# Optimization experiments

Hardware: AMD Instinct MI355X
Metric: run time of the kernel (lower is better)

Reference implementation:

```python
import jax, jax.numpy as jnp
import numpy as np

B, N, D = 4, 4096, 1024

def setup_inputs() -> dict:
    key = jax.random.key(0)
    kx, kql, kqr, kk, kv = jax.random.split(key, 5)
    std = 1.0 / D
    return {
        "x": jax.random.normal(kx, (B, N, D), dtype=jnp.float32),
        "w_query_left": jax.random.normal(kql, (D, D), dtype=jnp.float32) * std,
        "w_query_right": jax.random.normal(kqr, (D, D), dtype=jnp.float32) * std,
        "w_key": jax.random.normal(kk, (D, D), dtype=jnp.float32) * std,
        "w_value": jax.random.normal(kv, (D, D), dtype=jnp.float32) * std,
    }

def reference(x, w_query_left, w_query_right, w_key, w_value):
    # Four dxd projections
    query_left = jnp.einsum('bnd,de->bne', x, w_query_left)
    query_right = jnp.einsum('bnd,de->bne', x, w_query_right)
    key = jnp.einsum('bnd,de->bne', x, w_key)
    value = jnp.einsum('bnd,de->bne', x, w_value)
    # Elementwise gate
    query = query_left * query_right
    # Kernelized attention: key^T @ value, then query @ kv  (dropout p=0 in eval)
    kv_attn = jnp.einsum('bnd,bne->bde', key, value)   # [B, D, D]
    linear_attn = jnp.einsum('bnd,bde->bne', query, kv_attn)
    return linear_attn
```

## Files before the change

kernel.cpp:

```cpp
#include <hip/hip_runtime.h>
#include <stdint.h>

typedef short bf16x8 __attribute__((ext_vector_type(8)));
typedef float f32x4 __attribute__((ext_vector_type(4)));

__device__ __forceinline__ uint16_t f2b(float f) {
    uint32_t u = __builtin_bit_cast(uint32_t, f);
    return (uint16_t)((u + 0x7fffu + ((u >> 16) & 1u)) >> 16);
}

__device__ __forceinline__ void gll16(const void* g, void* l) {
    __builtin_amdgcn_global_load_lds(
        (const __attribute__((address_space(1))) uint32_t*)(uintptr_t)g,
        (__attribute__((address_space(3))) uint32_t*)(uint32_t)(uintptr_t)l,
        16, 0, 0);
}

__device__ __forceinline__ void swz3(int& bx, int& by, int& bz) {
    const int nx = gridDim.x, ny = gridDim.y, nz = gridDim.z;
    const int n = nx * ny * nz;
    int orig = blockIdx.x + nx * (blockIdx.y + ny * blockIdx.z);
    int l = (orig & 7) * (n >> 3) + (orig >> 3);
    bx = l % nx; l /= nx;
    by = l % ny;
    bz = l / ny;
}

struct Ptr4 { const float* p[4]; };

__global__ __launch_bounds__(256) void prep(const float* __restrict__ x,
                                            uint16_t* __restrict__ xb,
                                            uint16_t* __restrict__ xT,
                                            Ptr4 wp, uint16_t* __restrict__ Wt) {
    __shared__ uint16_t tile[64][68];
    const int t = threadIdx.x;
    int id = blockIdx.x;
    if (id < 4096) {
        const int d0 = (id & 15) * 64;
        const int n0 = ((id >> 4) & 63) * 64;
        const int b = id >> 10;
        const float* xbase = x + (size_t)b * 4194304;
#pragma unroll
        for (int p = 0; p < 4; p++) {
            int row = p * 16 + (t >> 4);
            int c4 = (t & 15) * 4;
            float4 v = *(const float4*)&xbase[(size_t)(n0 + row) * 1024 + d0 + c4];
            uint16_t b0 = f2b(v.x), b1 = f2b(v.y), b2 = f2b(v.z), b3 = f2b(v.w);
            tile[row][c4 + 0] = b0;
            tile[row][c4 + 1] = b1;
            tile[row][c4 + 2] = b2;
            tile[row][c4 + 3] = b3;
            uint2 pk;
            pk.x = (uint32_t)b0 | ((uint32_t)b1 << 16);
            pk.y = (uint32_t)b2 | ((uint32_t)b3 << 16);
            *(uint2*)&xb[(size_t)(b * 4096 + n0 + row) * 1024 + d0 + c4] = pk;
        }
        __syncthreads();
        uint16_t* oT = xT + (size_t)b * 4194304;
#pragma unroll
        for (int p = 0; p < 4; p++) {
            int a = p * 16 + (t >> 4);
            int b4 = (t & 15) * 4;
            uint32_t x0 = tile[b4 + 0][a], x1 = tile[b4 + 1][a];
            uint32_t x2 = tile[b4 + 2][a], x3 = tile[b4 + 3][a];
            uint2 pk;
            pk.x = x0 | (x1 << 16);
            pk.y = x2 | (x3 << 16);
            *(uint2*)&oT[(size_t)(d0 + a) * 4096 + n0 + b4] = pk;
        }
    } else {
        id -= 4096;
        const int c0 = (id & 15) * 64;
        const int r0 = ((id >> 4) & 15) * 64;
        const int m = id >> 8;
        const float* in = wp.p[m];
        uint16_t* o = Wt + (size_t)m * 1048576;
#pragma unroll
        for (int p = 0; p < 4; p++) {
            int row = p * 16 + (t >> 4);
            int c4 = (t & 15) * 4;
            float4 v = *(const float4*)&in[(size_t)(r0 + row) * 1024 + c0 + c4];
            tile[row][c4 + 0] = f2b(v.x);
            tile[row][c4 + 1] = f2b(v.y);
            tile[row][c4 + 2] = f2b(v.z);
            tile[row][c4 + 3] = f2b(v.w);
        }
        __syncthreads();
#pragma unroll
        for (int p = 0; p < 4; p++) {
            int a = p * 16 + (t >> 4);
            int b4 = (t & 15) * 4;
            uint32_t x0 = tile[b4 + 0][a], x1 = tile[b4 + 1][a];
            uint32_t x2 = tile[b4 + 2][a], x3 = tile[b4 + 3][a];
            uint2 pk;
            pk.x = x0 | (x1 << 16);
            pk.y = x2 | (x3 << 16);
            *(uint2*)&o[(size_t)(c0 + a) * 1024 + r0 + b4] = pk;
        }
    }
}

__global__ __launch_bounds__(512, 2) void proj_gate8(const uint16_t* __restrict__ A,
                                                     const uint16_t* __restrict__ Wt,
                                                     uint16_t* __restrict__ Q) {
    __shared__ uint16_t lds[65536];
    const int t = threadIdx.x;
    const int wave = t >> 6;
    const int lane = t & 63;
    int bx, by, bz;
    swz3(bx, by, bz);
    const int m0 = by * 256;
    const int e0 = bx * 128;
    const uint16_t* B1 = Wt + (size_t)e0 * 1024;
    const uint16_t* B2 = Wt + 1048576 + (size_t)e0 * 1024;
    const int wm = (wave >> 1) * 64;
    const int wn = (wave & 1) * 64;

    int LsA0 = t * 16;
    int LsA1 = 8192 + t * 16;
    int gbA0 = LsA0 ^ (((LsA0 >> 7) & 7) << 4);
    int gbA1 = LsA1 ^ (((LsA1 >> 7) & 7) << 4);
    int gbB  = LsA0 ^ (((LsA0 >> 7) & 7) << 4);
    const uint16_t* srcA0 = A + (size_t)(m0 + (gbA0 >> 6)) * 1024 + ((gbA0 & 63) >> 1);
    const uint16_t* srcA1 = A + (size_t)(m0 + (gbA1 >> 6)) * 1024 + ((gbA1 & 63) >> 1);
    const uint16_t* srcB1 = B1 + (size_t)(gbB >> 6) * 1024 + ((gbB & 63) >> 1);
    const uint16_t* srcB2 = B2 + (size_t)(gbB >> 6) * 1024 + ((gbB & 63) >> 1);

    auto STAGE = [&](int kt_, int ks_) {
        const int h = (2 * kt_ + ks_) & 3;
        const int kb = kt_ * 64 + ks_ * 32;
        uint16_t* db = lds + h * 16384 + (wave << 9);
        gll16(srcA0 + kb, db);
        gll16(srcA1 + kb, db + 4096);
        gll16(srcB1 + kb, db + 8192);
        gll16(srcB2 + kb, db + 12288);
    };

    const int cb = (lane >> 4) << 4;
    int aoff[4], b1off[4], b2off[4];
#pragma unroll
    for (int i = 0; i < 4; i++) {
        int g = (wm + i * 16 + (lane & 15)) * 64 + cb;
        aoff[i] = (g ^ (((g >> 7) & 7) << 4)) >> 1;
    }
#pragma unroll
    for (int j = 0; j < 4; j++) {
        int g = (wn + j * 16 + (lane & 15)) * 64 + cb;
        int sw = (g ^ (((g >> 7) & 7) << 4)) >> 1;
        b1off[j] = 8192 + sw;
        b2off[j] = 12288 + sw;
    }

    f32x4 acc1[4][4] = {};
    f32x4 acc2[4][4] = {};

    STAGE(0, 0); STAGE(0, 1); STAGE(1, 0); STAGE(1, 1);
    asm volatile("s_waitcnt vmcnt(12)" ::: "memory");
    __builtin_amdgcn_s_barrier();

    for (int kt = 0; kt < 16; ++kt) {
        const uint16_t* lb0 = lds + ((2 * kt) & 3) * 16384;
        const uint16_t* lb1 = lds + ((2 * kt + 1) & 3) * 16384;
        bf16x8 af[4], bq[4];

#pragma unroll
        for (int i = 0; i < 4; i++) af[i] = *(const bf16x8*)&lb0[aoff[i]];
#pragma unroll
        for (int j = 0; j < 4; j++) bq[j] = *(const bf16x8*)&lb0[b1off[j]];
        __builtin_amdgcn_s_barrier();
        asm volatile("s_waitcnt lgkmcnt(0)" ::: "memory");
        __builtin_amdgcn_sched_barrier(0);
        __builtin_amdgcn_s_setprio(1);
#pragma unroll
        for (int i = 0; i < 4; i++)
#pragma unroll
            for (int j = 0; j < 4; j++)
                acc1[i][j] = __builtin_amdgcn_mfma_f32_16x16x32_bf16(af[i], bq[j],
                                                                     acc1[i][j], 0, 0, 0);
        __builtin_amdgcn_s_setprio(0);
        __builtin_amdgcn_s_barrier();

#pragma unroll
        for (int j = 0; j < 4; j++) bq[j] = *(const bf16x8*)&lb0[b2off[j]];
        __builtin_amdgcn_s_barrier();
        asm volatile("s_waitcnt lgkmcnt(0)" ::: "memory");
        __builtin_amdgcn_sched_barrier(0);
        __builtin_amdgcn_s_setprio(1);
#pragma unroll
        for (int i = 0; i < 4; i++)
#pragma unroll
            for (int j = 0; j < 4; j++)
                acc2[i][j] = __builtin_amdgcn_mfma_f32_16x16x32_bf16(af[i], bq[j],
                                                                     acc2[i][j], 0, 0, 0);
        __builtin_amdgcn_s_setprio(0);
        if (kt < 15) { asm volatile("s_waitcnt vmcnt(8)" ::: "memory"); }
        else         { asm volatile("s_waitcnt vmcnt(0)" ::: "memory"); }
        __builtin_amdgcn_s_barrier();
        if (kt < 14) STAGE(kt + 2, 0);

#pragma unroll
        for (int i = 0; i < 4; i++) af[i] = *(const bf16x8*)&lb1[aoff[i]];
#pragma unroll
        for (int j = 0; j < 4; j++) bq[j] = *(const bf16x8*)&lb1[b1off[j]];
        __builtin_amdgcn_s_barrier();
        asm volatile("s_waitcnt lgkmcnt(0)" ::: "memory");
        __builtin_amdgcn_sched_barrier(0);
        __builtin_amdgcn_s_setprio(1);
#pragma unroll
        for (int i = 0; i < 4; i++)
#pragma unroll
            for (int j = 0; j < 4; j++)
                acc1[i][j] = __builtin_amdgcn_mfma_f32_16x16x32_bf16(af[i], bq[j],
                                                                     acc1[i][j], 0, 0, 0);
        __builtin_amdgcn_s_setprio(0);
        __builtin_amdgcn_s_barrier();

#pragma unroll
        for (int j = 0; j < 4; j++) bq[j] = *(const bf16x8*)&lb1[b2off[j]];
        __builtin_amdgcn_s_barrier();
        asm volatile("s_waitcnt lgkmcnt(0)" ::: "memory");
        __builtin_amdgcn_sched_barrier(0);
        __builtin_amdgcn_s_setprio(1);
#pragma unroll
        for (int i = 0; i < 4; i++)
#pragma unroll
            for (int j = 0; j < 4; j++)
                acc2[i][j] = __builtin_amdgcn_mfma_f32_16x16x32_bf16(af[i], bq[j],
                                                                     acc2[i][j], 0, 0, 0);
        __builtin_amdgcn_s_setprio(0);
        if (kt < 14)       { asm volatile("s_waitcnt vmcnt(8)" ::: "memory"); }
        else if (kt == 14) { asm volatile("s_waitcnt vmcnt(4)" ::: "memory"); }
        else               { asm volatile("s_waitcnt vmcnt(0)" ::: "memory"); }
        __builtin_amdgcn_s_barrier();
        if (kt < 14) STAGE(kt + 2, 1);
    }

    const int rl = (lane >> 4) * 4;
    const int cl = lane & 15;
#pragma unroll
    for (int i = 0; i < 4; i++)
#pragma unroll
        for (int j = 0; j < 4; j++)
#pragma unroll
            for (int r = 0; r < 4; r++) {
                float g = acc1[i][j][r] * acc2[i][j][r];
                Q[(size_t)(m0 + wm + i * 16 + rl + r) * 1024 + e0 + wn + j * 16 + cl] = f2b(g);
            }
}

__global__ __launch_bounds__(512, 2) void gemm_out8(const uint16_t* __restrict__ A,
                                                    const uint16_t* __restrict__ kvT,
                                                    float* __restrict__ C) {
    __shared__ uint16_t lds[65536];
    const int t = threadIdx.x;
    const int wave = t >> 6;
    const int lane = t & 63;
    int bx, by, bz;
    swz3(bx, by, bz);
    const int m0 = by * 256;
    const int n0 = bx * 256;
    const int batch = by >> 4;
    const uint16_t* Bb = kvT + (size_t)batch * 1048576 + (size_t)n0 * 1024;
    const int wm = (wave >> 2) * 128;
    const int wn = (wave & 3) * 64;

    int Ls0 = t * 16;
    int Ls1 = 8192 + t * 16;
    int gb0 = Ls0 ^ (((Ls0 >> 7) & 7) << 4);
    int gb1 = Ls1 ^ (((Ls1 >> 7) & 7) << 4);
    const uint16_t* srcA0 = A + (size_t)(m0 + (gb0 >> 6)) * 1024 + ((gb0 & 63) >> 1);
    const uint16_t* srcA1 = A + (size_t)(m0 + (gb1 >> 6)) * 1024 + ((gb1 & 63) >> 1);
    const uint16_t* srcB0 = Bb + (size_t)(gb0 >> 6) * 1024 + ((gb0 & 63) >> 1);
    const uint16_t* srcB1 = Bb + (size_t)(gb1 >> 6) * 1024 + ((gb1 & 63) >> 1);

    auto STAGE = [&](int kt_, int ks_) {
        const int h = (2 * kt_ + ks_) & 3;
        const int kb = kt_ * 64 + ks_ * 32;
        uint16_t* db = lds + h * 16384 + (wave << 9);
        gll16(srcA0 + kb, db);
        gll16(srcA1 + kb, db + 4096);
        gll16(srcB0 + kb, db + 8192);
        gll16(srcB1 + kb, db + 12288);
    };

    const int cb = (lane >> 4) << 4;
    int aoff[8], boff[4];
#pragma unroll
    for (int i = 0; i < 8; i++) {
        int g = (wm + i * 16 + (lane & 15)) * 64 + cb;
        aoff[i] = (g ^ (((g >> 7) & 7) << 4)) >> 1;
    }
#pragma unroll
    for (int j = 0; j < 4; j++) {
        int g = (wn + j * 16 + (lane & 15)) * 64 + cb;
        boff[j] = 8192 + ((g ^ (((g >> 7) & 7) << 4)) >> 1);
    }

    f32x4 acc[8][4] = {};

    STAGE(0, 0); STAGE(0, 1); STAGE(1, 0); STAGE(1, 1);
    asm volatile("s_waitcnt vmcnt(12)" ::: "memory");
    __builtin_amdgcn_s_barrier();

    for (int kt = 0; kt < 16; ++kt) {
        const uint16_t* lb0 = lds + ((2 * kt) & 3) * 16384;
        const uint16_t* lb1 = lds + ((2 * kt + 1) & 3) * 16384;
        bf16x8 af[8], bq[4];

#pragma unroll
        for (int i = 0; i < 8; i++) af[i] = *(const bf16x8*)&lb0[aoff[i]];
#pragma unroll
        for (int j = 0; j < 4; j++) bq[j] = *(const bf16x8*)&lb0[boff[j]];
        __builtin_amdgcn_s_barrier();
        asm volatile("s_waitcnt lgkmcnt(0)" ::: "memory");
        __builtin_amdgcn_sched_barrier(0);
        __builtin_amdgcn_s_setprio(1);
#pragma unroll
        for (int i = 0; i < 8; i++)
#pragma unroll
            for (int j = 0; j < 4; j++)
                acc[i][j] = __builtin_amdgcn_mfma_f32_16x16x32_bf16(af[i], bq[j],
                                                                    acc[i][j], 0, 0, 0);
        __builtin_amdgcn_s_setprio(0);
        if (kt < 15) { asm volatile("s_waitcnt vmcnt(8)" ::: "memory"); }
        else         { asm volatile("s_waitcnt vmcnt(0)" ::: "memory"); }
        __builtin_amdgcn_s_barrier();
        if (kt < 14) STAGE(kt + 2, 0);

#pragma unroll
        for (int i = 0; i < 8; i++) af[i] = *(const bf16x8*)&lb1[aoff[i]];
#pragma unroll
        for (int j = 0; j < 4; j++) bq[j] = *(const bf16x8*)&lb1[boff[j]];
        __builtin_amdgcn_s_barrier();
        asm volatile("s_waitcnt lgkmcnt(0)" ::: "memory");
        __builtin_amdgcn_sched_barrier(0);
        __builtin_amdgcn_s_setprio(1);
#pragma unroll
        for (int i = 0; i < 8; i++)
#pragma unroll
            for (int j = 0; j < 4; j++)
                acc[i][j] = __builtin_amdgcn_mfma_f32_16x16x32_bf16(af[i], bq[j],
                                                                    acc[i][j], 0, 0, 0);
        __builtin_amdgcn_s_setprio(0);
        if (kt < 14)       { asm volatile("s_waitcnt vmcnt(8)" ::: "memory"); }
        else if (kt == 14) { asm volatile("s_waitcnt vmcnt(4)" ::: "memory"); }
        else               { asm volatile("s_waitcnt vmcnt(0)" ::: "memory"); }
        __builtin_amdgcn_s_barrier();
        if (kt < 14) STAGE(kt + 2, 1);
    }

    const int rl = (lane >> 4) * 4;
    const int cl = lane & 15;
#pragma unroll
    for (int i = 0; i < 8; i++)
#pragma unroll
        for (int j = 0; j < 4; j++)
#pragma unroll
            for (int r = 0; r < 4; r++)
                C[(size_t)(m0 + wm + i * 16 + rl + r) * 1024 + n0 + wn + j * 16 + cl] =
                    acc[i][j][r];
}

__global__ __launch_bounds__(256) void gemm_kv_splitk(const uint16_t* __restrict__ VT,
                                                      const uint16_t* __restrict__ KT,
                                                      float* __restrict__ P) {
    int bxs, bys, bzs;
    swz3(bxs, bys, bzs);
    const int z = bzs;
    const int batch = z >> 1, ks = z & 1;
    const uint16_t* Ab = VT + (size_t)batch * 4194304 + ks * 2048;
    const uint16_t* Bb = KT + (size_t)batch * 4194304 + ks * 2048;

    __shared__ uint16_t lA[4096];
    __shared__ uint16_t lB[4096];

    const int t = threadIdx.x;
    const int wave = t >> 6;
    const int lane = t & 63;
    const int m0 = bys * 128;
    const int n0 = bxs * 128;
    const int wm = (wave >> 1) * 64;
    const int wn = (wave & 1) * 64;

    const uint16_t* gA0 = Ab + (size_t)(m0 + (t >> 2)) * 4096 + (t & 3) * 8;
    const uint16_t* gB0 = Bb + (size_t)(n0 + (t >> 2)) * 4096 + (t & 3) * 8;
    uint16_t* lA0 = lA + wave * 512;
    uint16_t* lA1 = lA + 2048 + wave * 512;
    uint16_t* lB0 = lB + wave * 512;
    uint16_t* lB1 = lB + 2048 + wave * 512;

    f32x4 acc[4][4] = {};

    const int arow = wm + (lane & 15);
    const int brow = wn + (lane & 15);
    const int koff = (lane >> 4) * 8;

    for (int k0 = 0; k0 < 2048; k0 += 32) {
        __syncthreads();
        gll16(gA0 + k0, lA0);
        gll16(gA0 + (size_t)64 * 4096 + k0, lA1);
        gll16(gB0 + k0, lB0);
        gll16(gB0 + (size_t)64 * 4096 + k0, lB1);
        __syncthreads();

        bf16x8 af[4], bfr[4];
#pragma unroll
        for (int i = 0; i < 4; i++)
            af[i] = *(const bf16x8*)&lA[(arow + i * 16) * 32 + koff];
#pragma unroll
        for (int i = 0; i < 4; i++)
            bfr[i] = *(const bf16x8*)&lB[(brow + i * 16) * 32 + koff];
#pragma unroll
        for (int i = 0; i < 4; i++)
#pragma unroll
            for (int j = 0; j < 4; j++)
                acc[i][j] = __builtin_amdgcn_mfma_f32_16x16x32_bf16(af[i], bfr[j],
                                                                    acc[i][j], 0, 0, 0);
    }

    float* Pb = P + (size_t)z * 1048576;
    const int crow = m0 + wm + (lane >> 4) * 4;
    const int ccol = n0 + wn + (lane & 15);
#pragma unroll
    for (int i = 0; i < 4; i++)
#pragma unroll
        for (int j = 0; j < 4; j++)
#pragma unroll
            for (int r = 0; r < 4; r++)
                Pb[(size_t)(crow + i * 16 + r) * 1024 + ccol + j * 16] = acc[i][j][r];
}

__global__ __launch_bounds__(256) void reduce_kv(const float4* __restrict__ P,
                                                 uint2* __restrict__ G) {
    int i = blockIdx.x * 256 + threadIdx.x;
    int b = i >> 18;
    int r = i & 262143;
    const float4* base = P + (size_t)b * 524288 + r;
    float4 s0 = base[0];
    float4 s1 = base[262144];
    float x = s0.x + s1.x;
    float y = s0.y + s1.y;
    float zz = s0.z + s1.z;
    float w = s0.w + s1.w;
    uint2 o;
    o.x = (uint32_t)f2b(x) | ((uint32_t)f2b(y) << 16);
    o.y = (uint32_t)f2b(zz) | ((uint32_t)f2b(w) << 16);
    G[i] = o;
}

__global__ __launch_bounds__(256) void gemm_nt_bf16(const uint16_t* __restrict__ A,
                                                    int lda, int az,
                                                    const uint16_t* __restrict__ Bt,
                                                    int ldb,
                                                    uint16_t* __restrict__ C,
                                                    int ldc, int cz) {
    int bxs, bys, bzs;
    swz3(bxs, bys, bzs);
    const uint16_t* Ab = A + (size_t)bzs * az;
    uint16_t* Cb = C + (size_t)bzs * cz;

    __shared__ uint16_t lA[4096];
    __shared__ uint16_t lB[4096];

    const int t = threadIdx.x;
    const int wave = t >> 6;
    const int lane = t & 63;
    const int m0 = bys * 128;
    const int n0 = bxs * 128;
    const int wm = (wave >> 1) * 64;
    const int wn = (wave & 1) * 64;

    const uint16_t* gA0 = Ab + (size_t)(m0 + (t >> 2)) * lda + (t & 3) * 8;
    const uint16_t* gB0 = Bt + (size_t)(n0 + (t >> 2)) * ldb + (t & 3) * 8;
    uint16_t* lA0 = lA + wave * 512;
    uint16_t* lA1 = lA + 2048 + wave * 512;
    uint16_t* lB0 = lB + wave * 512;
    uint16_t* lB1 = lB + 2048 + wave * 512;

    f32x4 acc[4][4] = {};

    const int arow = wm + (lane & 15);
    const int brow = wn + (lane & 15);
    const int koff = (lane >> 4) * 8;

    for (int k0 = 0; k0 < 1024; k0 += 32) {
        __syncthreads();
        gll16(gA0 + k0, lA0);
        gll16(gA0 + (size_t)64 * lda + k0, lA1);
        gll16(gB0 + k0, lB0);
        gll16(gB0 + (size_t)64 * ldb + k0, lB1);
        __syncthreads();

        bf16x8 af[4], bfr[4];
#pragma unroll
        for (int i = 0; i < 4; i++)
            af[i] = *(const bf16x8*)&lA[(arow + i * 16) * 32 + koff];
#pragma unroll
        for (int i = 0; i < 4; i++)
            bfr[i] = *(const bf16x8*)&lB[(brow + i * 16) * 32 + koff];
#pragma unroll
        for (int i = 0; i < 4; i++)
#pragma unroll
            for (int j = 0; j < 4; j++)
                acc[i][j] = __builtin_amdgcn_mfma_f32_16x16x32_bf16(af[i], bfr[j],
                                                                    acc[i][j], 0, 0, 0);
    }

    const int crow = m0 + wm + (lane >> 4) * 4;
    const int ccol = n0 + wn + (lane & 15);
#pragma unroll
    for (int i = 0; i < 4; i++)
#pragma unroll
        for (int j = 0; j < 4; j++)
#pragma unroll
            for (int r = 0; r < 4; r++)
                Cb[(size_t)(crow + i * 16 + r) * ldc + ccol + j * 16] = f2b(acc[i][j][r]);
}

extern "C" void kernel_launch(void* const* d_in, const int* in_sizes, int n_in,
                              void* d_out, int out_size, void* d_ws, size_t ws_size,
                              hipStream_t stream) {
    const float* x = (const float*)d_in[0];

    uint16_t* ws  = (uint16_t*)d_ws;
    uint16_t* xb  = ws;
    uint16_t* xT  = ws + 16777216;
    uint16_t* Wt  = ws + 33554432;
    uint16_t* Q   = ws + 37748736;
    float*    P   = (float*)(ws + 54525952);
    uint16_t* G   = ws + 71303168;
    uint16_t* H   = ws + 75497472;
    uint16_t* kvT = ws + 79691776;

    Ptr4 wp;
    wp.p[0] = (const float*)d_in[1];
    wp.p[1] = (const float*)d_in[2];
    wp.p[2] = (const float*)d_in[3];
    wp.p[3] = (const float*)d_in[4];
    prep<<<5120, 256, 0, stream>>>(x, xb, xT, wp, Wt);

    proj_gate8<<<dim3(8, 64), 512, 0, stream>>>(xb, Wt, Q);

    gemm_kv_splitk<<<dim3(8, 8, 8), 256, 0, stream>>>(xT, xT, P);

    reduce_kv<<<4096, 256, 0, stream>>>((const float4*)P, (uint2*)G);

    gemm_nt_bf16<<<dim3(32, 8, 1), 256, 0, stream>>>(Wt + 3 * 1048576, 1024, 0,
                                                     G, 1024, H, 4096, 0);

    gemm_nt_bf16<<<dim3(8, 8, 4), 256, 0, stream>>>(H, 4096, 1024,
                                                    Wt + 2 * 1048576, 1024,
                                                    kvT, 1024, 1048576);

    gemm_out8<<<dim3(4, 64), 512, 0, stream>>>(Q, kvT, (float*)d_out);
}
```

Measured before the change: 351.3 us.

## Pipeline Gram split-K GEMM and fuse partial reduction into H GEMM

Replaces the simple single-buffered split-K Gram kernel with an 8-wave, 4-stage pipelined kernel that uses swizzled LDS, global_load_lds prefetch and MFMA priority hints. It also removes the separate reduce kernel: the H GEMM now reads the two fp32 split-K partials directly, sums them, converts to bf16 and writes to LDS while loading its B operand. This cuts one launch and a round trip through the intermediate G buffer, but gemm_h loads the B operand through registers with synchronous fp32 loads, which could stall that GEMM.

```diff
diff --git a/kernel.cpp b/kernel.cpp
--- a/kernel.cpp
+++ b/kernel.cpp
@@ -120,7 +120,7 @@
     int LsA1 = 8192 + t * 16;
     int gbA0 = LsA0 ^ (((LsA0 >> 7) & 7) << 4);
     int gbA1 = LsA1 ^ (((LsA1 >> 7) & 7) << 4);
-    int gbB  = LsA0 ^ (((LsA0 >> 7) & 7) << 4);
+    int gbB  = gbA0;
     const uint16_t* srcA0 = A + (size_t)(m0 + (gbA0 >> 6)) * 1024 + ((gbA0 & 63) >> 1);
     const uint16_t* srcA1 = A + (size_t)(m0 + (gbA1 >> 6)) * 1024 + ((gbA1 & 63) >> 1);
     const uint16_t* srcB1 = B1 + (size_t)(gbB >> 6) * 1024 + ((gbB & 63) >> 1);
@@ -246,6 +246,206 @@
                 float g = acc1[i][j][r] * acc2[i][j][r];
                 Q[(size_t)(m0 + wm + i * 16 + rl + r) * 1024 + e0 + wn + j * 16 + cl] = f2b(g);
             }
+}
+
+__global__ __launch_bounds__(512, 2) void gram8(const uint16_t* __restrict__ xT,
+                                                float* __restrict__ P) {
+    __shared__ uint16_t lds[49152];
+    const int t = threadIdx.x;
+    const int wave = t >> 6;
+    const int lane = t & 63;
+    int bx, by, bz;
+    swz3(bx, by, bz);
+    const int m0 = by * 256;
+    const int n0 = bx * 128;
+    const int batch = bz >> 1, ks = bz & 1;
+    const uint16_t* Xb = xT + (size_t)batch * 4194304 + ks * 2048;
+    const int wm = (wave >> 1) * 64;
+    const int wn = (wave & 1) * 64;
+
+    int LsA0 = t * 16;
+    int LsA1 = 8192 + t * 16;
+    int gbA0 = LsA0 ^ (((LsA0 >> 7) & 7) << 4);
+    int gbA1 = LsA1 ^ (((LsA1 >> 7) & 7) << 4);
+    int gbB  = gbA0;
+    const uint16_t* srcA0 = Xb + (size_t)(m0 + (gbA0 >> 6)) * 4096 + ((gbA0 & 63) >> 1);
+    const uint16_t* srcA1 = Xb + (size_t)(m0 + (gbA1 >> 6)) * 4096 + ((gbA1 & 63) >> 1);
+    const uint16_t* srcB  = Xb + (size_t)(n0 + (gbB  >> 6)) * 4096 + ((gbB  & 63) >> 1);
+
+    auto STAGE = [&](int kt_, int ks2_) {
+        const int h = (2 * kt_ + ks2_) & 3;
+        const int kb = kt_ * 64 + ks2_ * 32;
+        uint16_t* db = lds + h * 12288 + (wave << 9);
+        gll16(srcA0 + kb, db);
+        gll16(srcA1 + kb, db + 4096);
+        gll16(srcB  + kb, db + 8192);
+    };
+
+    const int cb = (lane >> 4) << 4;
+    int aoff[4], boff[4];
+#pragma unroll
+    for (int i = 0; i < 4; i++) {
+        int g = (wm + i * 16 + (lane & 15)) * 64 + cb;
+        aoff[i] = (g ^ (((g >> 7) & 7) << 4)) >> 1;
+    }
+#pragma unroll
+    for (int j = 0; j < 4; j++) {
+        int g = (wn + j * 16 + (lane & 15)) * 64 + cb;
+        boff[j] = 8192 + ((g ^ (((g >> 7) & 7) << 4)) >> 1);
+    }
+
+    f32x4 acc[4][4] = {};
+
+    STAGE(0, 0); STAGE(0, 1); STAGE(1, 0); STAGE(1, 1);
+    asm volatile("s_waitcnt vmcnt(9)" ::: "memory");
+    __builtin_amdgcn_s_barrier();
+
+    for (int kt = 0; kt < 32; ++kt) {
+        const uint16_t* lb0 = lds + ((2 * kt) & 3) * 12288;
+        const uint16_t* lb1 = lds + ((2 * kt + 1) & 3) * 12288;
+        bf16x8 af[4], bq[4];
+
+#pragma unroll
+        for (int i = 0; i < 4; i++) af[i] = *(const bf16x8*)&lb0[aoff[i]];
+#pragma unroll
+        for (int j = 0; j < 4; j++) bq[j] = *(const bf16x8*)&lb0[boff[j]];
+        __builtin_amdgcn_s_barrier();
+        asm volatile("s_waitcnt lgkmcnt(0)" ::: "memory");
+        __builtin_amdgcn_sched_barrier(0);
+        __builtin_amdgcn_s_setprio(1);
+#pragma unroll
+        for (int i = 0; i < 4; i++)
+#pragma unroll
+            for (int j = 0; j < 4; j++)
+                acc[i][j] = __builtin_amdgcn_mfma_f32_16x16x32_bf16(af[i], bq[j],
+                                                                    acc[i][j], 0, 0, 0);
+        __builtin_amdgcn_s_setprio(0);
+        if (kt < 31) { asm volatile("s_waitcnt vmcnt(6)" ::: "memory"); }
+        else         { asm volatile("s_waitcnt vmcnt(0)" ::: "memory"); }
+        __builtin_amdgcn_s_barrier();
+        if (kt < 30) STAGE(kt + 2, 0);
+
+#pragma unroll
+        for (int i = 0; i < 4; i++) af[i] = *(const bf16x8*)&lb1[aoff[i]];
+#pragma unroll
+        for (int j = 0; j < 4; j++) bq[j] = *(const bf16x8*)&lb1[boff[j]];
+        __builtin_amdgcn_s_barrier();
+        asm volatile("s_waitcnt lgkmcnt(0)" ::: "memory");
+        __builtin_amdgcn_sched_barrier(0);
+        __builtin_amdgcn_s_setprio(1);
+#pragma unroll
+        for (int i = 0; i < 4; i++)
+#pragma unroll
+            for (int j = 0; j < 4; j++)
+                acc[i][j] = __builtin_amdgcn_mfma_f32_16x16x32_bf16(af[i], bq[j],
+                                                                    acc[i][j], 0, 0, 0);
+        __builtin_amdgcn_s_setprio(0);
+        if (kt < 30)       { asm volatile("s_waitcnt vmcnt(6)" ::: "memory"); }
+        else if (kt == 30) { asm volatile("s_waitcnt vmcnt(3)" ::: "memory"); }
+        else               { asm volatile("s_waitcnt vmcnt(0)" ::: "memory"); }
+        __builtin_amdgcn_s_barrier();
+        if (kt < 30) STAGE(kt + 2, 1);
+    }
+
+    float* Pb = P + (size_t)bz * 1048576;
+    const int crow = m0 + wm + (lane >> 4) * 4;
+    const int ccol = n0 + wn + (lane & 15);
+#pragma unroll
+    for (int i = 0; i < 4; i++)
+#pragma unroll
+        for (int j = 0; j < 4; j++)
+#pragma unroll
+            for (int r = 0; r < 4; r++)
+                Pb[(size_t)(crow + i * 16 + r) * 1024 + ccol + j * 16] = acc[i][j][r];
+}
+
+__global__ __launch_bounds__(256) void gemm_h(const uint16_t* __restrict__ WvT,
+                                              const float* __restrict__ P,
+                                              uint16_t* __restrict__ H) {
+    int bxs, bys, bzs;
+    swz3(bxs, bys, bzs);
+    __shared__ uint16_t lA[4096];
+    __shared__ uint16_t lB[4096];
+
+    const int t = threadIdx.x;
+    const int wave = t >> 6;
+    const int lane = t & 63;
+    const int m0 = bys * 128;
+    const int n0 = bxs * 128;
+    const int wm = (wave >> 1) * 64;
+    const int wn = (wave & 1) * 64;
+
+    const uint16_t* gA0 = WvT + (size_t)(m0 + (t >> 2)) * 1024 + (t & 3) * 8;
+    uint16_t* lA0 = lA + wave * 512;
+    uint16_t* lA1 = lA + 2048 + wave * 512;
+
+    const int row1 = n0 + (t >> 2);
+    const int row2 = row1 + 64;
+    const float* pb1 = P + (size_t)(row1 >> 10) * 2097152 + (size_t)(row1 & 1023) * 1024 + (t & 3) * 8;
+    const float* pb2 = P + (size_t)(row2 >> 10) * 2097152 + (size_t)(row2 & 1023) * 1024 + (t & 3) * 8;
+    uint16_t* wB1 = lB + (t >> 2) * 32 + (t & 3) * 8;
+    uint16_t* wB2 = lB + 2048 + (t >> 2) * 32 + (t & 3) * 8;
+
+    f32x4 acc[4][4] = {};
+
+    const int arow = wm + (lane & 15);
+    const int brow = wn + (lane & 15);
+    const int koff = (lane >> 4) * 8;
+
+    for (int k0 = 0; k0 < 1024; k0 += 32) {
+        __syncthreads();
+        gll16(gA0 + k0, lA0);
+        gll16(gA0 + (size_t)64 * 1024 + k0, lA1);
+        {
+            float4 a0 = *(const float4*)(pb1 + k0);
+            float4 a1 = *(const float4*)(pb1 + k0 + 4);
+            float4 b0 = *(const float4*)(pb1 + 1048576 + k0);
+            float4 b1 = *(const float4*)(pb1 + 1048576 + k0 + 4);
+            uint4 v;
+            v.x = (uint32_t)f2b(a0.x + b0.x) | ((uint32_t)f2b(a0.y + b0.y) << 16);
+            v.y = (uint32_t)f2b(a0.z + b0.z) | ((uint32_t)f2b(a0.w + b0.w) << 16);
+            v.z = (uint32_t)f2b(a1.x + b1.x) | ((uint32_t)f2b(a1.y + b1.y) << 16);
+            v.w = (uint32_t)f2b(a1.z + b1.z) | ((uint32_t)f2b(a1.w + b1.w) << 16);
+            *(uint4*)wB1 = v;
+        }
+        {
+            float4 a0 = *(const float4*)(pb2 + k0);
+            float4 a1 = *(const float4*)(pb2 + k0 + 4);
+            float4 b0 = *(const float4*)(pb2 + 1048576 + k0);
+            float4 b1 = *(const float4*)(pb2 + 1048576 + k0 + 4);
+            uint4 v;
+            v.x = (uint32_t)f2b(a0.x + b0.x) | ((uint32_t)f2b(a0.y + b0.y) << 16);
+            v.y = (uint32_t)f2b(a0.z + b0.z) | ((uint32_t)f2b(a0.w + b0.w) << 16);
+            v.z = (uint32_t)f2b(a1.x + b1.x) | ((uint32_t)f2b(a1.y + b1.y) << 16);
+            v.w = (uint32_t)f2b(a1.z + b1.z) | ((uint32_t)f2b(a1.w + b1.w) << 16);
+            *(uint4*)wB2 = v;
+        }
+        __syncthreads();
+
+        bf16x8 af[4], bfr[4];
+#pragma unroll
+        for (int i = 0; i < 4; i++)
+            af[i] = *(const bf16x8*)&lA[(arow + i * 16) * 32 + koff];
+#pragma unroll
+        for (int i = 0; i < 4; i++)
+            bfr[i] = *(const bf16x8*)&lB[(brow + i * 16) * 32 + koff];
+#pragma unroll
+        for (int i = 0; i < 4; i++)
+#pragma unroll
+            for (int j = 0; j < 4; j++)
+                acc[i][j] = __builtin_amdgcn_mfma_f32_16x16x32_bf16(af[i], bfr[j],
+                                                                    acc[i][j], 0, 0, 0);
+    }
+
+    const int crow = m0 + wm + (lane >> 4) * 4;
+    const int ccol = n0 + wn + (lane & 15);
+#pragma unroll
+    for (int i = 0; i < 4; i++)
+#pragma unroll
+        for (int j = 0; j < 4; j++)
+#pragma unroll
+            for (int r = 0; r < 4; r++)
+                H[(size_t)(crow + i * 16 + r) * 4096 + ccol + j * 16] = f2b(acc[i][j][r]);
 }
 
 __global__ __launch_bounds__(512, 2) void gemm_out8(const uint16_t* __restrict__ A,
@@ -361,93 +561,6 @@
                     acc[i][j][r];
 }
 
-__global__ __launch_bounds__(256) void gemm_kv_splitk(const uint16_t* __restrict__ VT,
-                                                      const uint16_t* __restrict__ KT,
-                                                      float* __restrict__ P) {
-    int bxs, bys, bzs;
-    swz3(bxs, bys, bzs);
-    const int z = bzs;
-    const int batch = z >> 1, ks = z & 1;
-    const uint16_t* Ab = VT + (size_t)batch * 4194304 + ks * 2048;
-    const uint16_t* Bb = KT + (size_t)batch * 4194304 + ks * 2048;
-
-    __shared__ uint16_t lA[4096];
-    __shared__ uint16_t lB[4096];
-
-    const int t = threadIdx.x;
-    const int wave = t >> 6;
-    const int lane = t & 63;
-    const int m0 = bys * 128;
-    const int n0 = bxs * 128;
-    const int wm = (wave >> 1) * 64;
-    const int wn = (wave & 1) * 64;
-
-    const uint16_t* gA0 = Ab + (size_t)(m0 + (t >> 2)) * 4096 + (t & 3) * 8;
-    const uint16_t* gB0 = Bb + (size_t)(n0 + (t >> 2)) * 4096 + (t & 3) * 8;
-    uint16_t* lA0 = lA + wave * 512;
-    uint16_t* lA1 = lA + 2048 + wave * 512;
-    uint16_t* lB0 = lB + wave * 512;
-    uint16_t* lB1 = lB + 2048 + wave * 512;
-
-    f32x4 acc[4][4] = {};
-
-    const int arow = wm + (lane & 15);
-    const int brow = wn + (lane & 15);
-    const int koff = (lane >> 4) * 8;
-
-    for (int k0 = 0; k0 < 2048; k0 += 32) {
-        __syncthreads();
-        gll16(gA0 + k0, lA0);
-        gll16(gA0 + (size_t)64 * 4096 + k0, lA1);
-        gll16(gB0 + k0, lB0);
-        gll16(gB0 + (size_t)64 * 4096 + k0, lB1);
-        __syncthreads();
-
-        bf16x8 af[4], bfr[4];
-#pragma unroll
-        for (int i = 0; i < 4; i++)
-            af[i] = *(const bf16x8*)&lA[(arow + i * 16) * 32 + koff];
-#pragma unroll
-        for (int i = 0; i < 4; i++)
-            bfr[i] = *(const bf16x8*)&lB[(brow + i * 16) * 32 + koff];
-#pragma unroll
-        for (int i = 0; i < 4; i++)
-#pragma unroll
-            for (int j = 0; j < 4; j++)
-                acc[i][j] = __builtin_amdgcn_mfma_f32_16x16x32_bf16(af[i], bfr[j],
-                                                                    acc[i][j], 0, 0, 0);
-    }
-
-    float* Pb = P + (size_t)z * 1048576;
-    const int crow = m0 + wm + (lane >> 4) * 4;
-    const int ccol = n0 + wn + (lane & 15);
-#pragma unroll
-    for (int i = 0; i < 4; i++)
-#pragma unroll
-        for (int j = 0; j < 4; j++)
-#pragma unroll
-            for (int r = 0; r < 4; r++)
-                Pb[(size_t)(crow + i * 16 + r) * 1024 + ccol + j * 16] = acc[i][j][r];
-}
-
-__global__ __launch_bounds__(256) void reduce_kv(const float4* __restrict__ P,
-                                                 uint2* __restrict__ G) {
-    int i = blockIdx.x * 256 + threadIdx.x;
-    int b = i >> 18;
-    int r = i & 262143;
-    const float4* base = P + (size_t)b * 524288 + r;
-    float4 s0 = base[0];
-    float4 s1 = base[262144];
-    float x = s0.x + s1.x;
-    float y = s0.y + s1.y;
-    float zz = s0.z + s1.z;
-    float w = s0.w + s1.w;
-    uint2 o;
-    o.x = (uint32_t)f2b(x) | ((uint32_t)f2b(y) << 16);
-    o.y = (uint32_t)f2b(zz) | ((uint32_t)f2b(w) << 16);
-    G[i] = o;
-}
-
 __global__ __launch_bounds__(256) void gemm_nt_bf16(const uint16_t* __restrict__ A,
                                                     int lda, int az,
                                                     const uint16_t* __restrict__ Bt,
@@ -528,7 +641,6 @@
     uint16_t* Wt  = ws + 33554432;
     uint16_t* Q   = ws + 37748736;
     float*    P   = (float*)(ws + 54525952);
-    uint16_t* G   = ws + 71303168;
     uint16_t* H   = ws + 75497472;
     uint16_t* kvT = ws + 79691776;
 
@@ -541,12 +653,9 @@
 
     proj_gate8<<<dim3(8, 64), 512, 0, stream>>>(xb, Wt, Q);
 
-    gemm_kv_splitk<<<dim3(8, 8, 8), 256, 0, stream>>>(xT, xT, P);
-
-    reduce_kv<<<4096, 256, 0, stream>>>((const float4*)P, (uint2*)G);
-
-    gemm_nt_bf16<<<dim3(32, 8, 1), 256, 0, stream>>>(Wt + 3 * 1048576, 1024, 0,
-                                                     G, 1024, H, 4096, 0);
+    gram8<<<dim3(8, 4, 8), 512, 0, stream>>>(xT, P);
+
+    gemm_h<<<dim3(32, 8, 1), 256, 0, stream>>>(Wt + 3 * 1048576, P, H);
 
     gemm_nt_bf16<<<dim3(8, 8, 4), 256, 0, stream>>>(H, 4096, 1024,
                                                     Wt + 2 * 1048576, 1024,
```

Result: no change. 352.3 us (+0.3%).
